# Kernel optimization log

Hardware: AMD Instinct MI355X
Metric: run time of the kernel (lower is better)

Reference implementation:

```python
import jax, jax.numpy as jnp
import numpy as np

DN = ('NCHW', 'OIHW', 'NCHW')

def conv2d(x, w, b, pad):
    y = jax.lax.conv_general_dilated(x, w, (1, 1), [(pad, pad), (pad, pad)], dimension_numbers=DN)
    return y + b[None, :, None, None]

def setup_inputs() -> dict:
    key = jax.random.key(0)
    ks = jax.random.split(key, 12)
    nc, hc = 10, 16
    B, H, W = 8, 256, 256
    s = 0.1  # small init scale
    return {
        'x': jax.random.normal(ks[0], (B, nc, H, W), dtype=jnp.float32),
        'perceive_w': jax.random.normal(ks[1], (hc * 2, nc + hc, 3, 3), dtype=jnp.float32) * s,
        'perceive_b': jax.random.normal(ks[2], (hc * 2,), dtype=jnp.float32) * s,
        'update1_w': jax.random.normal(ks[3], (hc, hc * 2, 1, 1), dtype=jnp.float32) * s,
        'update1_b': jax.random.normal(ks[4], (hc,), dtype=jnp.float32) * s,
        'update2_w': jax.random.normal(ks[5], (hc, hc, 1, 1), dtype=jnp.float32) * s,
        'update2_b': jax.random.normal(ks[6], (hc,), dtype=jnp.float32) * s,
        'tau_w': jax.random.normal(ks[7], (hc, nc + hc * 2, 3, 3), dtype=jnp.float32) * s,
        'tau_b': jax.random.normal(ks[8], (hc,), dtype=jnp.float32) * s,
        'b_tau': jnp.ones((1, hc, 1, 1), dtype=jnp.float32) * 1.5,
        'readout_w': jax.random.normal(ks[9], (nc, hc, 1, 1), dtype=jnp.float32) * s,
        'readout_b': jax.random.normal(ks[10], (nc,), dtype=jnp.float32) * s,
        'n_steps': 10,
    }

def reference(x, perceive_w, perceive_b, update1_w, update1_b, update2_w, update2_b,
              tau_w, tau_b, b_tau, readout_w, readout_b, n_steps):
    B, _, H, W = x.shape
    hc = update2_w.shape[0]
    state0 = jnp.zeros((B, hc, H, W), dtype=x.dtype)

    def step(state, _):
        combined = jnp.concatenate([x, state], axis=1)          # [B, nc+hc, H, W]
        perception = conv2d(combined, perceive_w, perceive_b, 1)  # [B, 2*hc, H, W]
        hidden = jax.nn.relu(conv2d(perception, update1_w, update1_b, 0))
        delta = conv2d(hidden, update2_w, update2_b, 0)          # [B, hc, H, W]
        tau_input = jnp.concatenate([x, state, delta], axis=1)   # [B, nc+2*hc, H, W]
        beta = jax.nn.sigmoid(conv2d(tau_input, tau_w, tau_b, 1) + b_tau)
        beta = jnp.clip(beta, 0.01, 0.99)
        state = beta * state + (1.0 - beta) * delta
        return state, None

    state, _ = jax.lax.scan(step, state0, None, length=n_steps)
    return conv2d(state, readout_w, readout_b, 0)                # [B, nc, H, W]
```

## Files before the change

### kernel.cpp

```cpp
#include <hip/hip_runtime.h>
#include <math.h>

#define BATCH 8
#define NC 10
#define HC 16
#define HH 256
#define WW 256
#define NSTEPS 10
#define PLANE (HH*WW)

typedef _Float16 v8h  __attribute__((ext_vector_type(8)));
typedef _Float16 v4h  __attribute__((ext_vector_type(4)));
typedef float    v16f __attribute__((ext_vector_type(16)));

#define TW 32
#define TH 8
#define IPW 36
#define IPH 12
#define IPOS (IPW*IPH)
#define ICH 40
#define DPW 34
#define DPH 10
#define DPOS (DPW*DPH)
#define DCH 24

#define MFMA32(A,B,C) __builtin_amdgcn_mfma_f32_32x32x16_f16(A, B, C, 0, 0, 0)

__global__ __launch_bounds__(256) void k_prep(
    const float* __restrict__ x, _Float16* __restrict__ xh)
{
    int g = blockIdx.x * 256 + threadIdx.x;
    int b = g >> 16, pix = g & 65535;
    v8h lo = {0,0,0,0,0,0,0,0}, hi = {0,0,0,0,0,0,0,0};
    #pragma unroll
    for (int c = 0; c < 8; ++c) lo[c] = (_Float16)x[(b*NC + c)*PLANE + pix];
    hi[0] = (_Float16)x[(b*NC + 8)*PLANE + pix];
    hi[1] = (_Float16)x[(b*NC + 9)*PLANE + pix];
    v8h* dst = (v8h*)&xh[(size_t)g * 16];
    dst[0] = lo; dst[1] = hi;
}

__global__ __launch_bounds__(256) void k_repack(
    const float* __restrict__ pw,
    const float* __restrict__ tw,
    const float* __restrict__ u1w, const float* __restrict__ u1b,
    const float* __restrict__ pb,
    const float* __restrict__ u2w,
    _Float16* __restrict__ apD,
    _Float16* __restrict__ apT,
    _Float16* __restrict__ apU1,
    _Float16* __restrict__ apU2,
    float* __restrict__ u1bp)
{
    const int tid = threadIdx.x;
    for (int i = tid; i < 9*2*512; i += 256) {
        int j = i & 7, lane = (i >> 3) & 63, kc = (i >> 9) & 1, t = i >> 10;
        int m = lane & 31, ke = (lane >> 5)*8 + j;
        float v = 0.f;
        if (kc == 1)      v = pw[(m*26 + 10 + ke)*9 + t];
        else if (ke < 10) v = pw[(m*26 + ke)*9 + t];
        apD[i] = (_Float16)v;
    }
    for (int i = tid; i < 9*3*512; i += 256) {
        int j = i & 7, lane = (i >> 3) & 63, r = i >> 9;
        int kc = r % 3, t = r / 3;
        int m = lane & 31, ke = (lane >> 5)*8 + j;
        float v = 0.f;
        if (m < 16) {
            if (kc == 0)      { if (ke < 10) v = tw[(m*42 + ke)*9 + t]; }
            else if (kc == 1) v = tw[(m*42 + 10 + ke)*9 + t];
            else              v = tw[(m*42 + 26 + ke)*9 + t];
        }
        apT[i] = (_Float16)v;
    }
    for (int i = tid; i < 2*2*512; i += 256) {
        int j = i & 7, lane = (i >> 3) & 63, part = (i >> 9) & 1, c = (i >> 10) & 1;
        int m = lane & 31, hh = lane >> 5;
        int ch = 16*c + 4*hh + (j & 3) + 8*(j >> 2);
        float w = (m < 16) ? u1w[m*32 + ch] : 0.f;
        _Float16 hi = (_Float16)w;
        apU1[i] = part ? (_Float16)(w - (float)hi) : hi;
    }
    for (int i = tid; i < 2*512; i += 256) {
        int j = i & 7, lane = (i >> 3) & 63, part = i >> 9;
        int m = lane & 31, hh = lane >> 5;
        int ch = 4*hh + (j & 3) + 8*(j >> 2);
        float w = (m < 16) ? u2w[m*16 + ch] : 0.f;
        _Float16 hi = (_Float16)w;
        apU2[i] = part ? (_Float16)(w - (float)hi) : hi;
    }
    if (tid < 16) {
        float s = u1b[tid];
        for (int p = 0; p < 32; ++p) s += u1w[tid*32 + p] * pb[p];
        u1bp[tid] = s;
    }
}

__device__ __forceinline__ void chain_mfma(
    const v16f A, int p, int h, int by, int bx,
    v8h u1h0, v8h u1r0, v8h u1h1, v8h u1r1,
    v8h u2h, v8h u2r,
    const float* bu1, const float* bu2,
    _Float16* __restrict__ smDl)
{
    v8h b0h, b1h;
    #pragma unroll
    for (int j = 0; j < 8; ++j) {
        b0h[j] = (_Float16)A[j];
        b1h[j] = (_Float16)A[8 + j];
    }
    v16f hacc = {0,0,0,0,0,0,0,0,0,0,0,0,0,0,0,0};
    hacc = MFMA32(u1h0, b0h, hacc);
    hacc = MFMA32(u1r0, b0h, hacc);
    hacc = MFMA32(u1h1, b1h, hacc);
    hacc = MFMA32(u1r1, b1h, hacc);
    v8h ch_;
    #pragma unroll
    for (int j = 0; j < 8; ++j)
        ch_[j] = (_Float16)fmaxf(hacc[j] + bu1[j], 0.f);
    v16f dacc = {0,0,0,0,0,0,0,0,0,0,0,0,0,0,0,0};
    dacc = MFMA32(u2h, ch_, dacc);
    dacc = MFMA32(u2r, ch_, dacc);

    const int yy = p / DPW, xx = p - yy * DPW;
    const int gy = by + yy - 1, gx = bx + xx - 1;
    const bool inImg = (gy >= 0 && gy < HH && gx >= 0 && gx < WW);

    v4h hi0, hi1;
    #pragma unroll
    for (int j = 0; j < 4; ++j) {
        float d0 = inImg ? (dacc[j]     + bu2[j])     : 0.f;
        float d1 = inImg ? (dacc[4 + j] + bu2[4 + j]) : 0.f;
        hi0[j] = (_Float16)d0;
        hi1[j] = (_Float16)d1;
    }
    _Float16* dst = &smDl[p * DCH];
    *(v4h*)(dst + 4*h)     = hi0;
    *(v4h*)(dst + 8 + 4*h) = hi1;
}

__global__ __launch_bounds__(256, 3) void k_step(
    const _Float16* __restrict__ xh,
    const _Float16* __restrict__ shO,
    const _Float16* __restrict__ apD,
    const _Float16* __restrict__ apT,
    const _Float16* __restrict__ apU1,
    const _Float16* __restrict__ apU2,
    const float* __restrict__ u1bp, const float* __restrict__ u2b,
    const float* __restrict__ tb,  const float* __restrict__ btau,
    _Float16* __restrict__ shN,
    const float* __restrict__ rw,  const float* __restrict__ rb,
    float* __restrict__ out, int first, int last)
{
    __shared__ __align__(16) _Float16 smIn[IPOS * ICH];
    __shared__ __align__(16) _Float16 smDl[DPOS * DCH];

    const int tid = threadIdx.x;

    int lin = blockIdx.x + 8*(blockIdx.y + 32*blockIdx.z);
    lin = (lin & 7)*256 + (lin >> 3);
    const int bx = (lin & 7) * TW;
    const int by = ((lin >> 3) & 31) * TH;
    const int b  = lin >> 8;

    for (int i = tid; i < IPOS; i += 256) {
        int yy = i / IPW, xx = i - yy * IPW;
        int gy = by + yy - 2, gx = bx + xx - 2;
        v8h x0 = {0,0,0,0,0,0,0,0}, x1 = x0, s0 = x0, s1 = x0;
        if (gy >= 0 && gy < HH && gx >= 0 && gx < WW) {
            size_t base = ((size_t)((b*HH + gy)*WW + gx)) * 16;
            const v8h* px_ = (const v8h*)&xh[base];
            x0 = px_[0]; x1 = px_[1];
            if (!first) {
                const v8h* ps_ = (const v8h*)&shO[base];
                s0 = ps_[0]; s1 = ps_[1];
            }
        }
        _Float16* d = &smIn[i * ICH];
        *(v8h*)(d)      = x0;  *(v8h*)(d + 8)  = x1;
        *(v8h*)(d + 16) = s0;  *(v8h*)(d + 24) = s1;
    }

    const int lane = tid & 63, w = tid >> 6;
    const int n = lane & 31, h = lane >> 5;

    v8h u1f00 = *(const v8h*)&apU1[(0*2 + 0)*512 + lane*8];
    v8h u1f01 = *(const v8h*)&apU1[(0*2 + 1)*512 + lane*8];
    v8h u1f10 = *(const v8h*)&apU1[(1*2 + 0)*512 + lane*8];
    v8h u1f11 = *(const v8h*)&apU1[(1*2 + 1)*512 + lane*8];
    v8h u2fh  = *(const v8h*)&apU2[0*512 + lane*8];
    v8h u2fr  = *(const v8h*)&apU2[1*512 + lane*8];
    float bu1[8], bu2[8], btAdd[8];
    #pragma unroll
    for (int j = 0; j < 8; ++j) {
        int m = (j & 3) + 8*(j >> 2) + 4*h;
        bu1[j] = u1bp[m];
        bu2[j] = u2b[m];
        btAdd[j] = tb[m] + btau[m];
    }
    __syncthreads();

    v16f acc0 = {0,0,0,0,0,0,0,0,0,0,0,0,0,0,0,0};
    v16f acc1 = acc0, acc2 = acc0;
    int pA = w*32 + n;           if (pA > DPOS-1) pA = DPOS-1;
    int pB = (w+4)*32 + n;       if (pB > DPOS-1) pB = DPOS-1;
    int pC = (w+8)*32 + n;       if (pC > DPOS-1) pC = DPOS-1;
    const bool hasC = (w < 3);
    int yyA = pA / DPW, xxA = pA - yyA*DPW;
    int yyB = pB / DPW, xxB = pB - yyB*DPW;
    int yyC = pC / DPW, xxC = pC - yyC*DPW;
    int adA = (yyA*IPW + xxA)*(ICH*2) + h*16;
    int adB = (yyB*IPW + xxB)*(ICH*2) + h*16;
    int adC = (yyC*IPW + xxC)*(ICH*2) + h*16;
    const char* smInB = (const char*)smIn;

    #pragma unroll
    for (int t = 0; t < 9; ++t) {
        const int dy = t / 3, dx = t - dy*3;
        const int off = (dy*IPW + dx)*(ICH*2);
        v8h A0 = *(const v8h*)&apD[(t*2 + 0)*512 + lane*8];
        v8h A1 = *(const v8h*)&apD[(t*2 + 1)*512 + lane*8];
        v8h bb;
        bb = *(const v8h*)(smInB + adA + off);      acc0 = MFMA32(A0, bb, acc0);
        bb = *(const v8h*)(smInB + adA + off + 32); acc0 = MFMA32(A1, bb, acc0);
        bb = *(const v8h*)(smInB + adB + off);      acc1 = MFMA32(A0, bb, acc1);
        bb = *(const v8h*)(smInB + adB + off + 32); acc1 = MFMA32(A1, bb, acc1);
        if (hasC) {
            bb = *(const v8h*)(smInB + adC + off);      acc2 = MFMA32(A0, bb, acc2);
            bb = *(const v8h*)(smInB + adC + off + 32); acc2 = MFMA32(A1, bb, acc2);
        }
    }

    chain_mfma(acc0, pA, h, by, bx, u1f00, u1f01, u1f10, u1f11, u2fh, u2fr, bu1, bu2, smDl);
    chain_mfma(acc1, pB, h, by, bx, u1f00, u1f01, u1f10, u1f11, u2fh, u2fr, bu1, bu2, smDl);
    if (hasC)
        chain_mfma(acc2, pC, h, by, bx, u1f00, u1f01, u1f10, u1f11, u2fh, u2fr, bu1, bu2, smDl);
    __syncthreads();

    v8h tA[27];
    #pragma unroll
    for (int t = 0; t < 9; ++t) {
        tA[t*3 + 0] = *(const v8h*)&apT[(t*3 + 0)*512 + lane*8];
        tA[t*3 + 1] = *(const v8h*)&apT[(t*3 + 1)*512 + lane*8];
        tA[t*3 + 2] = *(const v8h*)&apT[(t*3 + 2)*512 + lane*8];
    }

    v16f tc0 = {0,0,0,0,0,0,0,0,0,0,0,0,0,0,0,0};
    v16f tc1 = tc0;
    const int tt0 = w*2, tt1 = w*2 + 1;
    int adI0 = ((tt0 + 1)*IPW + (n + 1))*(ICH*2) + h*16;
    int adI1 = ((tt1 + 1)*IPW + (n + 1))*(ICH*2) + h*16;
    int adD0 = (tt0*DPW + n)*(DCH*2) + h*16;
    int adD1 = (tt1*DPW + n)*(DCH*2) + h*16;
    const char* smDlB = (const char*)smDl;

    #pragma unroll
    for (int t = 0; t < 9; ++t) {
        const int dy = t / 3, dx = t - dy*3;
        const int offI = (dy*IPW + dx)*(ICH*2);
        const int offD = (dy*DPW + dx)*(DCH*2);
        v8h bb;
        bb = *(const v8h*)(smInB + adI0 + offI);      tc0 = MFMA32(tA[t*3+0], bb, tc0);
        bb = *(const v8h*)(smInB + adI0 + offI + 32); tc0 = MFMA32(tA[t*3+1], bb, tc0);
        bb = *(const v8h*)(smDlB + adD0 + offD);      tc0 = MFMA32(tA[t*3+2], bb, tc0);
        bb = *(const v8h*)(smInB + adI1 + offI);      tc1 = MFMA32(tA[t*3+0], bb, tc1);
        bb = *(const v8h*)(smInB + adI1 + offI + 32); tc1 = MFMA32(tA[t*3+1], bb, tc1);
        bb = *(const v8h*)(smDlB + adD1 + offD);      tc1 = MFMA32(tA[t*3+2], bb, tc1);
    }

    #pragma unroll
    for (int g2 = 0; g2 < 2; ++g2) {
        const v16f T = g2 ? tc1 : tc0;
        const int tt = g2 ? tt1 : tt0;
        const int gy = by + tt, gx = bx + n;
        const int dbase = ((tt + 1)*DPW + (n + 1)) * DCH;
        const int ibase = ((tt + 2)*IPW + (n + 2)) * ICH + 16;
        v4h dlv[2], sov[2];
        dlv[0] = *(const v4h*)&smDl[dbase + 4*h];
        dlv[1] = *(const v4h*)&smDl[dbase + 8 + 4*h];
        sov[0] = *(const v4h*)&smIn[ibase + 4*h];
        sov[1] = *(const v4h*)&smIn[ibase + 8 + 4*h];
        float snv[8];
        #pragma unroll
        for (int mb = 0; mb < 2; ++mb)
            #pragma unroll
            for (int i2 = 0; i2 < 4; ++i2) {
                const int j = mb*4 + i2;
                float v = T[j] + btAdd[j];
                float bt = 1.f / (1.f + __expf(-v));
                bt = fminf(fmaxf(bt, 0.01f), 0.99f);
                float dl = (float)dlv[mb][i2];
                float so = (float)sov[mb][i2];
                snv[j] = dl + bt*(so - dl);
            }
        if (!last) {
            size_t pb_ = ((size_t)((b*HH + gy)*WW + gx)) * 16;
            #pragma unroll
            for (int mb = 0; mb < 2; ++mb) {
                v4h q;
                q[0] = (_Float16)snv[mb*4+0]; q[1] = (_Float16)snv[mb*4+1];
                q[2] = (_Float16)snv[mb*4+2]; q[3] = (_Float16)snv[mb*4+3];
                *(v4h*)&shN[pb_ + mb*8 + 4*h] = q;
            }
        } else {
            float rcv[8];
            #pragma unroll
            for (int r = 0; r < 8; ++r) rcv[r] = __shfl_xor(snv[r], 32);
            if (h == 0) {
                #pragma unroll
                for (int o = 0; o < NC; ++o) {
                    float s = rb[o];
                    #pragma unroll
                    for (int mb = 0; mb < 2; ++mb)
                        #pragma unroll
                        for (int i2 = 0; i2 < 4; ++i2) {
                            s = fmaf(snv[mb*4+i2], rw[o*16 + mb*8 + i2],     s);
                            s = fmaf(rcv[mb*4+i2], rw[o*16 + mb*8 + 4 + i2], s);
                        }
                    out[((b*NC + o)*HH + gy)*WW + gx] = s;
                }
            }
        }
    }
}

extern "C" void kernel_launch(void* const* d_in, const int* in_sizes, int n_in,
                              void* d_out, int out_size, void* d_ws, size_t ws_size,
                              hipStream_t stream) {
    const float* x    = (const float*)d_in[0];
    const float* pw   = (const float*)d_in[1];
    const float* pb   = (const float*)d_in[2];
    const float* u1w  = (const float*)d_in[3];
    const float* u1b  = (const float*)d_in[4];
    const float* u2w  = (const float*)d_in[5];
    const float* u2b  = (const float*)d_in[6];
    const float* tw   = (const float*)d_in[7];
    const float* tb   = (const float*)d_in[8];
    const float* btau = (const float*)d_in[9];
    const float* rw   = (const float*)d_in[10];
    const float* rb   = (const float*)d_in[11];

    const size_t planeN = (size_t)BATCH * HC * PLANE;
    _Float16* shA  = (_Float16*)d_ws;
    _Float16* shB  = shA + planeN;
    _Float16* xhp  = shB + planeN;
    _Float16* apD  = xhp + planeN;
    _Float16* apT  = apD + 9*2*512;
    _Float16* apU1 = apT + 9*3*512;
    _Float16* apU2 = apU1 + 2*2*512;
    float*    u1bp = (float*)(apU2 + 2*512);


    k_prep<<<BATCH * PLANE / 256, 256, 0, stream>>>(x, xhp);
    k_repack<<<1, 256, 0, stream>>>(pw, tw, u1w, u1b, pb, u2w, apD, apT, apU1, apU2, u1bp);

    dim3 blk(256);
    dim3 grd(WW / TW, HH / TH, BATCH);

    for (int step = 0; step < NSTEPS; ++step) {
        const bool even = (step % 2 == 0);
        const _Float16* shO = even ? shA : shB;
        _Float16*       shN = even ? shB : shA;
        k_step<<<grd, blk, 0, stream>>>(xhp, shO, apD, apT, apU1, apU2,
                                        u1bp, u2b, tb, btau,
                                        shN, rw, rb, (float*)d_out,
                                        step == 0 ? 1 : 0,
                                        step == NSTEPS - 1 ? 1 : 0);
    }
}
```

Measured before the change: 483.9 us.

## Read static x channels from padded global buffer instead of LDS staging

The fp16 copy of x is stored in a zero-padded 260x260 layout so the conv MFMA loops can fetch its B-fragments straight from global/L2 without bounds checks. Only the recurrent state is staged in shared memory now, which cuts per-block LDS from 40 to 24 channels and allows raising launch bounds to 4 blocks per CU. The cost is extra global loads in the inner MFMA loops, which depend on cache hits, plus a memset of the padded buffer.

```diff
diff --git a/kernel.cpp b/kernel.cpp
--- a/kernel.cpp
+++ b/kernel.cpp
@@ -8,6 +8,8 @@
 #define WW 256
 #define NSTEPS 10
 #define PLANE (HH*WW)
+#define PW 260
+#define PH 260
 
 typedef _Float16 v8h  __attribute__((ext_vector_type(8)));
 typedef _Float16 v4h  __attribute__((ext_vector_type(4)));
@@ -18,7 +20,7 @@
 #define IPW 36
 #define IPH 12
 #define IPOS (IPW*IPH)
-#define ICH 40
+#define ICH 24
 #define DPW 34
 #define DPH 10
 #define DPOS (DPW*DPH)
@@ -31,12 +33,13 @@
 {
     int g = blockIdx.x * 256 + threadIdx.x;
     int b = g >> 16, pix = g & 65535;
+    int gy = pix >> 8, gx = pix & 255;
     v8h lo = {0,0,0,0,0,0,0,0}, hi = {0,0,0,0,0,0,0,0};
     #pragma unroll
     for (int c = 0; c < 8; ++c) lo[c] = (_Float16)x[(b*NC + c)*PLANE + pix];
     hi[0] = (_Float16)x[(b*NC + 8)*PLANE + pix];
     hi[1] = (_Float16)x[(b*NC + 9)*PLANE + pix];
-    v8h* dst = (v8h*)&xh[(size_t)g * 16];
+    v8h* dst = (v8h*)&xh[(((size_t)b*PH + gy + 2)*PW + (gx + 2)) * 16];
     dst[0] = lo; dst[1] = hi;
 }
 
@@ -139,7 +142,7 @@
     *(v4h*)(dst + 8 + 4*h) = hi1;
 }
 
-__global__ __launch_bounds__(256, 3) void k_step(
+__global__ __launch_bounds__(256, 4) void k_step(
     const _Float16* __restrict__ xh,
     const _Float16* __restrict__ shO,
     const _Float16* __restrict__ apD,
@@ -166,19 +169,14 @@
     for (int i = tid; i < IPOS; i += 256) {
         int yy = i / IPW, xx = i - yy * IPW;
         int gy = by + yy - 2, gx = bx + xx - 2;
-        v8h x0 = {0,0,0,0,0,0,0,0}, x1 = x0, s0 = x0, s1 = x0;
-        if (gy >= 0 && gy < HH && gx >= 0 && gx < WW) {
+        v8h s0 = {0,0,0,0,0,0,0,0}, s1 = s0;
+        if (!first && gy >= 0 && gy < HH && gx >= 0 && gx < WW) {
             size_t base = ((size_t)((b*HH + gy)*WW + gx)) * 16;
-            const v8h* px_ = (const v8h*)&xh[base];
-            x0 = px_[0]; x1 = px_[1];
-            if (!first) {
-                const v8h* ps_ = (const v8h*)&shO[base];
-                s0 = ps_[0]; s1 = ps_[1];
-            }
+            const v8h* ps_ = (const v8h*)&shO[base];
+            s0 = ps_[0]; s1 = ps_[1];
         }
         _Float16* d = &smIn[i * ICH];
-        *(v8h*)(d)      = x0;  *(v8h*)(d + 8)  = x1;
-        *(v8h*)(d + 16) = s0;  *(v8h*)(d + 24) = s1;
+        *(v8h*)(d) = s0;  *(v8h*)(d + 8) = s1;
     }
 
     const int lane = tid & 63, w = tid >> 6;
@@ -198,10 +196,7 @@
         bu2[j] = u2b[m];
         btAdd[j] = tb[m] + btau[m];
     }
-    __syncthreads();
-
-    v16f acc0 = {0,0,0,0,0,0,0,0,0,0,0,0,0,0,0,0};
-    v16f acc1 = acc0, acc2 = acc0;
+
     int pA = w*32 + n;           if (pA > DPOS-1) pA = DPOS-1;
     int pB = (w+4)*32 + n;       if (pB > DPOS-1) pB = DPOS-1;
     int pC = (w+8)*32 + n;       if (pC > DPOS-1) pC = DPOS-1;
@@ -212,22 +207,30 @@
     int adA = (yyA*IPW + xxA)*(ICH*2) + h*16;
     int adB = (yyB*IPW + xxB)*(ICH*2) + h*16;
     int adC = (yyC*IPW + xxC)*(ICH*2) + h*16;
+    const _Float16* xbA = &xh[((size_t)(b*PH + by + yyA)*PW + (bx + xxA))*16 + h*8];
+    const _Float16* xbB = &xh[((size_t)(b*PH + by + yyB)*PW + (bx + xxB))*16 + h*8];
+    const _Float16* xbC = &xh[((size_t)(b*PH + by + yyC)*PW + (bx + xxC))*16 + h*8];
     const char* smInB = (const char*)smIn;
 
+    __syncthreads();
+
+    v16f acc0 = {0,0,0,0,0,0,0,0,0,0,0,0,0,0,0,0};
+    v16f acc1 = acc0, acc2 = acc0;
     #pragma unroll
     for (int t = 0; t < 9; ++t) {
         const int dy = t / 3, dx = t - dy*3;
         const int off = (dy*IPW + dx)*(ICH*2);
+        const int xoff = (dy*PW + dx)*16;
         v8h A0 = *(const v8h*)&apD[(t*2 + 0)*512 + lane*8];
         v8h A1 = *(const v8h*)&apD[(t*2 + 1)*512 + lane*8];
         v8h bb;
-        bb = *(const v8h*)(smInB + adA + off);      acc0 = MFMA32(A0, bb, acc0);
-        bb = *(const v8h*)(smInB + adA + off + 32); acc0 = MFMA32(A1, bb, acc0);
-        bb = *(const v8h*)(smInB + adB + off);      acc1 = MFMA32(A0, bb, acc1);
-        bb = *(const v8h*)(smInB + adB + off + 32); acc1 = MFMA32(A1, bb, acc1);
+        bb = *(const v8h*)&xbA[xoff];               acc0 = MFMA32(A0, bb, acc0);
+        bb = *(const v8h*)(smInB + adA + off);      acc0 = MFMA32(A1, bb, acc0);
+        bb = *(const v8h*)&xbB[xoff];               acc1 = MFMA32(A0, bb, acc1);
+        bb = *(const v8h*)(smInB + adB + off);      acc1 = MFMA32(A1, bb, acc1);
         if (hasC) {
-            bb = *(const v8h*)(smInB + adC + off);      acc2 = MFMA32(A0, bb, acc2);
-            bb = *(const v8h*)(smInB + adC + off + 32); acc2 = MFMA32(A1, bb, acc2);
+            bb = *(const v8h*)&xbC[xoff];           acc2 = MFMA32(A0, bb, acc2);
+            bb = *(const v8h*)(smInB + adC + off);  acc2 = MFMA32(A1, bb, acc2);
         }
     }
 
@@ -252,6 +255,8 @@
     int adI1 = ((tt1 + 1)*IPW + (n + 1))*(ICH*2) + h*16;
     int adD0 = (tt0*DPW + n)*(DCH*2) + h*16;
     int adD1 = (tt1*DPW + n)*(DCH*2) + h*16;
+    const _Float16* xbI0 = &xh[((size_t)(b*PH + by + tt0 + 1)*PW + (bx + n + 1))*16 + h*8];
+    const _Float16* xbI1 = &xh[((size_t)(b*PH + by + tt1 + 1)*PW + (bx + n + 1))*16 + h*8];
     const char* smDlB = (const char*)smDl;
 
     #pragma unroll
@@ -259,13 +264,14 @@
         const int dy = t / 3, dx = t - dy*3;
         const int offI = (dy*IPW + dx)*(ICH*2);
         const int offD = (dy*DPW + dx)*(DCH*2);
+        const int xoff = (dy*PW + dx)*16;
         v8h bb;
-        bb = *(const v8h*)(smInB + adI0 + offI);      tc0 = MFMA32(tA[t*3+0], bb, tc0);
-        bb = *(const v8h*)(smInB + adI0 + offI + 32); tc0 = MFMA32(tA[t*3+1], bb, tc0);
-        bb = *(const v8h*)(smDlB + adD0 + offD);      tc0 = MFMA32(tA[t*3+2], bb, tc0);
-        bb = *(const v8h*)(smInB + adI1 + offI);      tc1 = MFMA32(tA[t*3+0], bb, tc1);
-        bb = *(const v8h*)(smInB + adI1 + offI + 32); tc1 = MFMA32(tA[t*3+1], bb, tc1);
-        bb = *(const v8h*)(smDlB + adD1 + offD);      tc1 = MFMA32(tA[t*3+2], bb, tc1);
+        bb = *(const v8h*)&xbI0[xoff];            tc0 = MFMA32(tA[t*3+0], bb, tc0);
+        bb = *(const v8h*)(smInB + adI0 + offI);  tc0 = MFMA32(tA[t*3+1], bb, tc0);
+        bb = *(const v8h*)(smDlB + adD0 + offD);  tc0 = MFMA32(tA[t*3+2], bb, tc0);
+        bb = *(const v8h*)&xbI1[xoff];            tc1 = MFMA32(tA[t*3+0], bb, tc1);
+        bb = *(const v8h*)(smInB + adI1 + offI);  tc1 = MFMA32(tA[t*3+1], bb, tc1);
+        bb = *(const v8h*)(smDlB + adD1 + offD);  tc1 = MFMA32(tA[t*3+2], bb, tc1);
     }
 
     #pragma unroll
@@ -274,7 +280,7 @@
         const int tt = g2 ? tt1 : tt0;
         const int gy = by + tt, gx = bx + n;
         const int dbase = ((tt + 1)*DPW + (n + 1)) * DCH;
-        const int ibase = ((tt + 2)*IPW + (n + 2)) * ICH + 16;
+        const int ibase = ((tt + 2)*IPW + (n + 2)) * ICH;
         v4h dlv[2], sov[2];
         dlv[0] = *(const v4h*)&smDl[dbase + 4*h];
         dlv[1] = *(const v4h*)&smDl[dbase + 8 + 4*h];
@@ -341,15 +347,17 @@
     const float* rb   = (const float*)d_in[11];
 
     const size_t planeN = (size_t)BATCH * HC * PLANE;
+    const size_t xpadN  = (size_t)BATCH * PH * PW * 16;
     _Float16* shA  = (_Float16*)d_ws;
     _Float16* shB  = shA + planeN;
     _Float16* xhp  = shB + planeN;
-    _Float16* apD  = xhp + planeN;
+    _Float16* apD  = xhp + xpadN;
     _Float16* apT  = apD + 9*2*512;
     _Float16* apU1 = apT + 9*3*512;
     _Float16* apU2 = apU1 + 2*2*512;
     float*    u1bp = (float*)(apU2 + 2*512);
 
+    hipMemsetAsync(xhp, 0, xpadN * sizeof(_Float16), stream);
 
     k_prep<<<BATCH * PLANE / 256, 256, 0, stream>>>(x, xhp);
     k_repack<<<1, 256, 0, stream>>>(pw, tw, u1w, u1b, pb, u2w, apD, apT, apU1, apU2, u1bp);
```

After: 614.6 us. 1.27x slower.
